# Kernel tuning notes

Measured on AMD Instinct MI355X. Metric: run time of the kernel, lower is better.

The kernel has to match this reference:

```python
import jax, jax.numpy as jnp
import numpy as np

EMBED_DIM = 2048
NUM_HEADS = 16
NUM_HEADS_KV = 16
HEAD_DIM = EMBED_DIM // NUM_HEADS  # 128
ROT_DIM = HEAD_DIM // 2            # rotary_emb_dim = 64 (partial rotary)
ROPE_BASE = 10000.0
SEQLEN = 2048


def _rope_cos_sin(seqlen):
    # inv_freq over rotary dim (fp32 positions, as pos_idx_in_fp32=True)
    inv_freq = 1.0 / (ROPE_BASE ** (jnp.arange(0, ROT_DIM, 2, dtype=jnp.float32) / ROT_DIM))
    t = jnp.arange(seqlen, dtype=jnp.float32)
    freqs = jnp.outer(t, inv_freq)                 # (S, ROT_DIM//2)
    return jnp.cos(freqs), jnp.sin(freqs)


def _apply_rotary(x, cos, sin):
    # x: (B, S, H, D); non-interleaved (GPT-NeoX) rotary on first ROT_DIM dims
    rd = cos.shape[-1] * 2
    x_rot, x_pass = x[..., :rd], x[..., rd:]
    x1, x2 = x_rot[..., : rd // 2], x_rot[..., rd // 2 :]
    c = cos[None, :, None, :]
    s = sin[None, :, None, :]
    o1 = x1 * c - x2 * s
    o2 = x1 * s + x2 * c
    return jnp.concatenate([o1, o2, x_pass], axis=-1)


def setup_inputs() -> dict:
    key = jax.random.key(0)
    ks = jax.random.split(key, 5)
    scale_in = 1.0 / np.sqrt(EMBED_DIM)
    return {
        "x_q": jax.random.normal(ks[0], (SEQLEN, EMBED_DIM), dtype=jnp.float32),
        "Wqkv_w": jax.random.normal(ks[1], (HEAD_DIM * (NUM_HEADS + 2 * NUM_HEADS_KV), EMBED_DIM), dtype=jnp.float32) * scale_in,
        "Wqkv_b": jax.random.normal(ks[2], (HEAD_DIM * (NUM_HEADS + 2 * NUM_HEADS_KV),), dtype=jnp.float32) * 0.01,
        "Wo_w": jax.random.normal(ks[3], (EMBED_DIM, EMBED_DIM), dtype=jnp.float32) * scale_in,
        "Wo_b": jax.random.normal(ks[4], (EMBED_DIM,), dtype=jnp.float32) * 0.01,
    }


def reference(x_q, Wqkv_w, Wqkv_b, Wo_w, Wo_b):
    S = x_q.shape[0]
    H, Hkv, D = NUM_HEADS, NUM_HEADS_KV, HEAD_DIM
    # fused QKV projection
    qkv = x_q @ Wqkv_w.T + Wqkv_b                     # (S, (H+2Hkv)*D)
    q = qkv[:, : H * D].reshape(1, S, H, D)
    kv = qkv[:, H * D :].reshape(1, S, 2, Hkv, D)
    # rotary (q_position_ids = k_position_ids = arange(S))
    cos, sin = _rope_cos_sin(S)
    q = _apply_rotary(q, cos, sin)
    k = _apply_rotary(kv[:, :, 0], cos, sin)          # (1, S, Hkv, D)
    v = kv[:, :, 1]
    # causal attention, softmax scale 1/sqrt(D)
    scores = jnp.einsum("bshd,bthd->bhst", q, k) / jnp.sqrt(jnp.float32(D))
    causal = jnp.arange(S)[:, None] >= jnp.arange(S)[None, :]  # (S, S)
    scores = jnp.where(causal[None, None], scores, jnp.float32(-1e30))
    attn = jax.nn.softmax(scores, axis=-1)
    out = jnp.einsum("bhst,bthd->bshd", attn, v)      # (1, S, H, D)
    out = out.reshape(1, S, H * D)
    out = out @ Wo_w.T + Wo_b
    return out[0]                                     # (S, E)
```

## Files before the change

kernel.cpp:

```cpp
#include <hip/hip_runtime.h>
#include <stdint.h>

#define QKV_N 6144
#define ATT_SCALE 0.08838834764831845f

typedef __attribute__((ext_vector_type(8))) short short8;
typedef __attribute__((ext_vector_type(4))) float f32x4;

__device__ __forceinline__ uint16_t f2b(float x){
  uint32_t u = __float_as_uint(x);
  uint32_t r = (u + 0x7fffu + ((u >> 16) & 1u)) >> 16;
  return (uint16_t)r;
}
__device__ __forceinline__ float b2f(uint16_t h){
  return __uint_as_float(((uint32_t)h) << 16);
}
__device__ __forceinline__ void g2l16(const void* g, void* l){
  __builtin_amdgcn_global_load_lds((const __attribute__((address_space(1))) void*)g,
                                   (__attribute__((address_space(3))) void*)l, 16, 0, 0);
}

__device__ __forceinline__ void cvt8(const float* __restrict__ in, uint16_t* __restrict__ out, int i){
  const float4* p = (const float4*)in;
  float4 a = p[2*i], b = p[2*i+1];
  union { short8 v; uint16_t u[8]; } o;
  o.u[0]=f2b(a.x); o.u[1]=f2b(a.y); o.u[2]=f2b(a.z); o.u[3]=f2b(a.w);
  o.u[4]=f2b(b.x); o.u[5]=f2b(b.y); o.u[6]=f2b(b.z); o.u[7]=f2b(b.w);
  ((short8*)out)[i] = o.v;
}

__global__ __launch_bounds__(256) void k_prep(const float* __restrict__ x,
                                              const float* __restrict__ wqkv,
                                              const float* __restrict__ wo,
                                              uint16_t* __restrict__ xb,
                                              uint16_t* __restrict__ wqkvb,
                                              uint16_t* __restrict__ wob,
                                              float* __restrict__ ct,
                                              float* __restrict__ st){
  const int b = blockIdx.x, tid = threadIdx.x;
  if (b < 2048) {
    cvt8(x, xb, b*256 + tid);
  } else if (b < 8192) {
    cvt8(wqkv, wqkvb, (b - 2048)*256 + tid);
  } else if (b < 10240) {
    cvt8(wo, wob, (b - 8192)*256 + tid);
  } else {
    int i = (b - 10240)*256 + tid;
    int s = i >> 5, d = i & 31;
    float inv = __expf(-(float)d * (9.210340371976184f / 32.0f));
    float f = (float)s * inv;
    ct[i] = cosf(f);
    st[i] = sinf(f);
  }
}

__global__ __launch_bounds__(512, 1) void k_gemmA(const uint16_t* __restrict__ A,
                                                  const uint16_t* __restrict__ B,
                                                  const float* __restrict__ bias,
                                                  uint16_t* __restrict__ C){
  __shared__ uint16_t As[4*4096];
  __shared__ uint16_t Bs[4*12288];
  const int K = 2048, N = 6144;

  const int wg = blockIdx.x;
  const int xcd = wg & 7, bi = wg >> 3;
  const int m0 = (xcd*2 + (bi & 1)) * 128;
  const int n0 = (bi >> 1) * 384;

  const int tid = threadIdx.x;
  const int wid = tid >> 6, l = tid & 63;
  const int wm = wid >> 2, wn = wid & 3;
  const int g = l >> 4, c = l & 15;

  const int rp_s = tid >> 3;
  const int s_s  = (tid & 7) ^ (rp_s & 7);
  const size_t srcA0 = (size_t)(m0 + rp_s*2 + (s_s >> 2)) * K + (s_s & 3) * 8;
  const size_t srcB0 = (size_t)(n0 + rp_s*2 + (s_s >> 2)) * K + (s_s & 3) * 8;
  const size_t bstride = (size_t)128 * K;

  const int pg   = ((c & 1) << 2) | g;
  const int slb  = (pg ^ ((c >> 1) & 7)) << 3;
  const int rpa0 = wm*32 + (c >> 1);
  const int rpb0 = wn*48 + (c >> 1);

  f32x4 acc[4][6] = {};
  const int NT = K >> 5;

  #pragma unroll
  for (int t0 = 0; t0 < 3; ++t0) {
    g2l16(A + srcA0 + t0*32,             (void*)(As + t0*4096  + tid*8));
    g2l16(B + srcB0 + t0*32,             (void*)(Bs + t0*12288 + tid*8));
    g2l16(B + srcB0 + bstride + t0*32,   (void*)(Bs + t0*12288 + 4096 + tid*8));
    g2l16(B + srcB0 + 2*bstride + t0*32, (void*)(Bs + t0*12288 + 8192 + tid*8));
  }
  asm volatile("s_waitcnt vmcnt(8)" ::: "memory");
  __builtin_amdgcn_s_barrier();

  #pragma unroll 4
  for (int t = 0; t < NT; ++t) {
    const uint16_t* __restrict__ Ab = As + (t & 3)*4096;
    const uint16_t* __restrict__ Bb = Bs + (t & 3)*12288;
    const int t3 = t + 3;
    const bool pf = t3 < NT;
    const int a3 = (t3 & 3)*4096;
    const int b3 = (t3 & 3)*12288;

    short8 av[4], bv[3];
    #pragma unroll
    for (int mi = 0; mi < 4; ++mi)
      av[mi] = *(const short8*)&Ab[(rpa0 + mi*8)*64 + slb];
    #pragma unroll
    for (int ni = 0; ni < 3; ++ni)
      bv[ni] = *(const short8*)&Bb[(rpb0 + ni*8)*64 + slb];
    if (pf) {
      g2l16(A + srcA0 + t3*32, (void*)(As + a3 + tid*8));
      g2l16(B + srcB0 + t3*32, (void*)(Bs + b3 + tid*8));
    }
    __builtin_amdgcn_s_barrier();
    __builtin_amdgcn_s_setprio(1);
    #pragma unroll
    for (int mi = 0; mi < 4; ++mi)
      #pragma unroll
      for (int ni = 0; ni < 3; ++ni)
        acc[mi][ni] = __builtin_amdgcn_mfma_f32_16x16x32_bf16(av[mi], bv[ni], acc[mi][ni], 0, 0, 0);
    __builtin_amdgcn_s_setprio(0);
    __builtin_amdgcn_s_barrier();

    short8 bw[3];
    #pragma unroll
    for (int ni = 0; ni < 3; ++ni)
      bw[ni] = *(const short8*)&Bb[(rpb0 + (ni+3)*8)*64 + slb];
    if (pf) {
      g2l16(B + srcB0 + bstride + t3*32,   (void*)(Bs + b3 + 4096 + tid*8));
      g2l16(B + srcB0 + 2*bstride + t3*32, (void*)(Bs + b3 + 8192 + tid*8));
    }
    __builtin_amdgcn_s_barrier();
    __builtin_amdgcn_s_setprio(1);
    #pragma unroll
    for (int mi = 0; mi < 4; ++mi)
      #pragma unroll
      for (int ni = 0; ni < 3; ++ni)
        acc[mi][ni+3] = __builtin_amdgcn_mfma_f32_16x16x32_bf16(av[mi], bw[ni], acc[mi][ni+3], 0, 0, 0);
    __builtin_amdgcn_s_setprio(0);
    asm volatile("s_waitcnt vmcnt(8)" ::: "memory");
    __builtin_amdgcn_s_barrier();
  }

  #pragma unroll
  for (int ni = 0; ni < 6; ++ni) {
    const int col = n0 + wn*96 + ni*16 + c;
    const float bvl = bias[col];
    #pragma unroll
    for (int mi = 0; mi < 4; ++mi) {
      const int row0 = m0 + wm*64 + mi*16 + g*4;
      #pragma unroll
      for (int j = 0; j < 4; ++j)
        C[(size_t)(row0 + j)*N + col] = f2b(acc[mi][ni][j] + bvl);
    }
  }
}

__global__ __launch_bounds__(512, 1) void k_gemm128(const uint16_t* __restrict__ A,
                                                    const uint16_t* __restrict__ B,
                                                    const float* __restrict__ bias,
                                                    float* __restrict__ C,
                                                    int M, int N, int K){
  __shared__ uint16_t As[4*4096];
  __shared__ uint16_t Bs[4*4096];

  const int wg = blockIdx.x;
  const int xcd = wg & 7, bi = wg >> 3;
  const int m0 = (xcd*2 + (bi & 1)) * 128;
  const int n0 = (bi >> 1) * 128;

  const int tid = threadIdx.x;
  const int wid = tid >> 6, l = tid & 63;
  const int wm = wid >> 2, wn = wid & 3;
  const int g = l >> 4, c = l & 15;

  const int rp_s = tid >> 3, q_s = tid & 7, s_s = q_s ^ (rp_s & 7);
  const int srcA = (m0 + rp_s*2 + (s_s >> 2)) * K + (s_s & 3) * 8;
  const int srcB = (n0 + rp_s*2 + (s_s >> 2)) * K + (s_s & 3) * 8;

  const int pg  = ((c & 1) << 2) | g;
  const int slb = (pg ^ ((c >> 1) & 7)) << 3;
  const int ra0 = wm*32 + (c >> 1);
  const int rb0 = wn*16 + (c >> 1);

  f32x4 acc[4][2] = {};
  const int NT = K >> 5;

  #pragma unroll
  for (int t0 = 0; t0 < 3; ++t0) {
    g2l16(A + srcA + t0*32, (void*)(As + t0*4096 + tid*8));
    g2l16(B + srcB + t0*32, (void*)(Bs + t0*4096 + tid*8));
  }
  asm volatile("s_waitcnt vmcnt(4)" ::: "memory");
  __builtin_amdgcn_s_barrier();

  #pragma unroll 4
  for (int t = 0; t < NT; ++t) {
    const uint16_t* __restrict__ Ab = As + (t & 3)*4096;
    const uint16_t* __restrict__ Bb = Bs + (t & 3)*4096;
    const int t3 = t + 3;
    const int b3 = (t3 & 3)*4096;

    short8 av[4], bv[2];
    #pragma unroll
    for (int mi = 0; mi < 4; ++mi)
      av[mi] = *(const short8*)&Ab[(ra0 + mi*8)*64 + slb];
    #pragma unroll
    for (int ni = 0; ni < 2; ++ni)
      bv[ni] = *(const short8*)&Bb[(rb0 + ni*8)*64 + slb];
    if (t3 < NT) {
      g2l16(A + srcA + t3*32, (void*)(As + b3 + tid*8));
      g2l16(B + srcB + t3*32, (void*)(Bs + b3 + tid*8));
    }
    __builtin_amdgcn_s_barrier();
    __builtin_amdgcn_s_setprio(1);
    #pragma unroll
    for (int mi = 0; mi < 4; ++mi)
      #pragma unroll
      for (int ni = 0; ni < 2; ++ni)
        acc[mi][ni] = __builtin_amdgcn_mfma_f32_16x16x32_bf16(av[mi], bv[ni], acc[mi][ni], 0, 0, 0);
    __builtin_amdgcn_s_setprio(0);
    asm volatile("s_waitcnt vmcnt(4)" ::: "memory");
    __builtin_amdgcn_s_barrier();
  }

  #pragma unroll
  for (int ni = 0; ni < 2; ++ni) {
    const int col = n0 + wn*32 + ni*16 + c;
    const float bvl = bias[col];
    #pragma unroll
    for (int mi = 0; mi < 4; ++mi) {
      const int row0 = m0 + wm*64 + mi*16 + g*4;
      #pragma unroll
      for (int j = 0; j < 4; ++j)
        C[(size_t)(row0 + j)*N + col] = acc[mi][ni][j] + bvl;
    }
  }
}

__global__ __launch_bounds__(256) void k_rope_vt(const uint16_t* __restrict__ qkv,
                                                 const float* __restrict__ ct,
                                                 const float* __restrict__ st,
                                                 uint16_t* __restrict__ qo,
                                                 uint16_t* __restrict__ ko,
                                                 uint16_t* __restrict__ vt){
  const int blk = blockIdx.x, tid = threadIdx.x;
  if (blk < 4096) {
    int idx = blk * 256 + tid;
    int db = idx & 15;
    int s  = (idx >> 4) & 2047;
    int h  = (idx >> 15) & 15;
    int which = idx >> 19;
    const uint16_t* src = qkv + (size_t)s * QKV_N + which * 2048 + h * 128;
    uint16_t* dst = (which ? ko : qo) + (((size_t)(h*2048 + s)) << 7) + db*8;
    const float scale = which ? 1.0f : ATT_SCALE;
    int d0 = db * 8;
    union { short8 v; uint16_t u[8]; } o;
    if (d0 >= 64) {
      short8 xv = *(const short8*)(src + d0);
      #pragma unroll
      for (int e = 0; e < 8; ++e) o.u[e] = f2b(b2f((uint16_t)xv[e]) * scale);
    } else {
      int dd = d0 & 31;
      short8 a = *(const short8*)(src + dd);
      short8 b = *(const short8*)(src + dd + 32);
      float4 c0 = *(const float4*)(ct + s*32 + dd);
      float4 c1 = *(const float4*)(ct + s*32 + dd + 4);
      float4 s0 = *(const float4*)(st + s*32 + dd);
      float4 s1 = *(const float4*)(st + s*32 + dd + 4);
      float cc[8] = {c0.x,c0.y,c0.z,c0.w,c1.x,c1.y,c1.z,c1.w};
      float ss[8] = {s0.x,s0.y,s0.z,s0.w,s1.x,s1.y,s1.z,s1.w};
      #pragma unroll
      for (int e = 0; e < 8; ++e) {
        float x1 = b2f((uint16_t)a[e]), x2 = b2f((uint16_t)b[e]);
        float v = (d0 < 32) ? (x1*cc[e] - x2*ss[e]) : (x1*ss[e] + x2*cc[e]);
        o.u[e] = f2b(v * scale);
      }
    }
    *(short8*)dst = o.v;
  } else {
    __shared__ uint16_t tl[64][80];
    const int b = blk - 4096;
    const int st_ = b & 31, dt = (b >> 5) & 1, h = b >> 6;
    const int s_l = tid >> 2, cch = (tid & 3) * 16;
    const uint16_t* src = qkv + (size_t)(st_*64 + s_l) * QKV_N + 4096 + h*128 + dt*64 + cch;
    short8 a = *(const short8*)src;
    short8 b2 = *(const short8*)(src + 8);
    #pragma unroll
    for (int e = 0; e < 8; ++e) {
      tl[cch + e][s_l]     = (uint16_t)a[e];
      tl[cch + 8 + e][s_l] = (uint16_t)b2[e];
    }
    __syncthreads();
    const int d_l = tid >> 2;
    uint16_t* dst = vt + ((size_t)h << 18) + (size_t)(dt*64 + d_l) * 2048 + st_*64 + cch;
    *(short8*)dst       = *(const short8*)&tl[d_l][cch];
    *(short8*)(dst + 8) = *(const short8*)&tl[d_l][cch + 8];
  }
}

__global__ __launch_bounds__(512, 1) void k_attn(const uint16_t* __restrict__ Q,
                                                 const uint16_t* __restrict__ Kb,
                                                 const uint16_t* __restrict__ Vtg,
                                                 uint16_t* __restrict__ Out){
  __shared__ uint16_t Ks[2][2][64*128];
  __shared__ uint16_t Vs[2][2][128*64];
  __shared__ uint16_t Ps[8][16*88];

  const int bid = blockIdx.x;
  const int lin = (bid & 7) * 32 + (bid >> 3);
  const int h = lin >> 4;
  const int pair = lin & 15;

  const int tid = threadIdx.x, w = tid >> 6, l = tid & 63;
  const int gid = w >> 2, wq = w & 3;
  const int tg = tid & 255;
  const int g = l >> 4, c = l & 15;
  const int swz = (c & 7) << 4;

  const uint16_t* __restrict__ Qh = Q   + ((size_t)h << 18);
  const uint16_t* __restrict__ Kh = Kb  + ((size_t)h << 18);
  const uint16_t* __restrict__ Vh = Vtg + ((size_t)h << 18);
  float* scratch = (float*)&Ks[0][0][0];

  int koff[4], voff[4];
  #pragma unroll
  for (int j = 0; j < 4; ++j) {
    int kr = j*16 + (tg >> 4);
    koff[j] = kr*128 + (((tg & 15) ^ (kr & 7)) << 3);
    int vd = j*32 + (tg >> 3);
    voff[j] = vd*2048 + (((tg & 7) ^ (vd & 7)) << 3);
  }

  uint16_t* KsG = &Ks[gid][0][0];
  uint16_t* VsG = &Vs[gid][0][0];

  #pragma unroll 1
  for (int half = 0; half < 2; ++half) {
    const int qt = half ? (31 - pair) : pair;
    const int nt = qt + 1;
    const int nsteps = (nt + 1) >> 1;
    const int qrow = qt*64 + wq*16 + c;

    short8 qf[4];
    #pragma unroll
    for (int t = 0; t < 4; ++t)
      qf[t] = *(const short8*)&Qh[(size_t)qrow*128 + t*32 + g*8];

    f32x4 acc[8] = {};
    float mrow[4], lrow[4];
    #pragma unroll
    for (int j = 0; j < 4; ++j) { mrow[j] = -3e38f; lrow[j] = 0.0f; }

    if (gid < nt) {
      #pragma unroll
      for (int j = 0; j < 4; ++j) {
        g2l16(Kh + (size_t)gid*8192 + koff[j], (void*)(KsG + j*2048 + tg*8));
        g2l16(Vh + gid*64 + voff[j],           (void*)(VsG + j*2048 + tg*8));
      }
    }
    asm volatile("s_waitcnt vmcnt(0)" ::: "memory");
    __syncthreads();

    #pragma unroll 1
    for (int step = 0; step < nsteps; ++step) {
      const int kt = 2*step + gid;
      const int cur = step & 1;
      if (kt + 2 < nt) {
        const int k1 = kt + 2;
        #pragma unroll
        for (int j = 0; j < 4; ++j) {
          g2l16(Kh + (size_t)k1*8192 + koff[j], (void*)(KsG + (cur^1)*8192 + j*2048 + tg*8));
          g2l16(Vh + k1*64 + voff[j],           (void*)(VsG + (cur^1)*8192 + j*2048 + tg*8));
        }
      }

      if (kt < nt) {
        const int k0 = kt * 64;
        const uint16_t* Kcur = KsG + cur*8192;
        const uint16_t* Vcur = VsG + cur*8192;

        f32x4 sc4[4] = {};
        #pragma unroll
        for (int ct2 = 0; ct2 < 4; ++ct2) {
          const char* krp = (const char*)Kcur + (ct2*16 + c)*256;
          #pragma unroll
          for (int t = 0; t < 4; ++t) {
            short8 kb = *(const short8*)(krp + ((t*64 + g*16) ^ swz));
            sc4[ct2] = __builtin_amdgcn_mfma_f32_16x16x32_bf16(qf[t], kb, sc4[ct2], 0, 0, 0);
          }
        }

        const bool lastt = (kt == nt - 1);
        #pragma unroll
        for (int j = 0; j < 4; ++j) {
          const int qg = qt*64 + wq*16 + g*4 + j;
          float v0 = sc4[0][j], v1 = sc4[1][j], v2 = sc4[2][j], v3 = sc4[3][j];
          if (lastt) {
            if (k0 +      c > qg) v0 = -3e38f;
            if (k0 + 16 + c > qg) v1 = -3e38f;
            if (k0 + 32 + c > qg) v2 = -3e38f;
            if (k0 + 48 + c > qg) v3 = -3e38f;
          }
          float t0 = fmaxf(fmaxf(v0, v1), fmaxf(v2, v3));
          #pragma unroll
          for (int d2 = 1; d2 < 16; d2 <<= 1) t0 = fmaxf(t0, __shfl_xor(t0, d2, 64));
          const float mn = fmaxf(mrow[j], t0);
          const float scl = __expf(mrow[j] - mn);
          const float p0 = __expf(v0 - mn), p1 = __expf(v1 - mn),
                      p2 = __expf(v2 - mn), p3 = __expf(v3 - mn);
          float rs = (p0 + p1) + (p2 + p3);
          #pragma unroll
          for (int d2 = 1; d2 < 16; d2 <<= 1) rs += __shfl_xor(rs, d2, 64);
          lrow[j] = lrow[j]*scl + rs;
          mrow[j] = mn;
          #pragma unroll
          for (int n = 0; n < 8; ++n) acc[n][j] *= scl;
          uint16_t* pw = &Ps[w][(g*4 + j)*88];
          pw[c] = f2b(p0); pw[16+c] = f2b(p1); pw[32+c] = f2b(p2); pw[48+c] = f2b(p3);
        }

        #pragma unroll
        for (int kk = 0; kk < 2; ++kk) {
          short8 pf = *(const short8*)&Ps[w][c*88 + kk*32 + g*8];
          #pragma unroll
          for (int n = 0; n < 8; ++n) {
            const char* vrp = (const char*)Vcur + (n*16 + c)*128;
            short8 vf = *(const short8*)(vrp + ((kk*64 + g*16) ^ swz));
            acc[n] = __builtin_amdgcn_mfma_f32_16x16x32_bf16(pf, vf, acc[n], 0, 0, 0);
          }
        }
      }

      asm volatile("s_waitcnt vmcnt(0)" ::: "memory");
      __syncthreads();
    }

    float* Up = scratch + wq * 2112;
    if (gid == 1) {
      #pragma unroll
      for (int j = 0; j < 4; ++j) {
        const int row = g*4 + j;
        #pragma unroll
        for (int n = 0; n < 8; ++n)
          Up[row*128 + n*16 + c] = acc[n][j];
        if (c == 0) { Up[2048 + row] = mrow[j]; Up[2064 + row] = lrow[j]; }
      }
    }
    __syncthreads();
    if (gid == 0) {
      #pragma unroll
      for (int j = 0; j < 4; ++j) {
        const int row = g*4 + j;
        const int qg = qt*64 + wq*16 + row;
        const float mB = Up[2048 + row], lB = Up[2064 + row];
        const float mn = fmaxf(mrow[j], mB);
        const float e1 = __expf(mrow[j] - mn);
        const float e2 = __expf(mB - mn);
        const float inv = 1.0f / (lrow[j]*e1 + lB*e2);
        #pragma unroll
        for (int n = 0; n < 8; ++n) {
          const float u = acc[n][j]*e1 + Up[row*128 + n*16 + c]*e2;
          Out[(size_t)qg*2048 + h*128 + n*16 + c] = f2b(u * inv);
        }
      }
    }
    __syncthreads();
  }
}

extern "C" void kernel_launch(void* const* d_in, const int* in_sizes, int n_in,
                              void* d_out, int out_size, void* d_ws, size_t ws_size,
                              hipStream_t stream){
  const float* x    = (const float*)d_in[0];
  const float* Wqkv = (const float*)d_in[1];
  const float* bqkv = (const float*)d_in[2];
  const float* Wo   = (const float*)d_in[3];
  const float* bo   = (const float*)d_in[4];

  char* ws = (char*)d_ws;
  uint16_t* q_bf    = (uint16_t*)(ws);
  uint16_t* k_bf    = (uint16_t*)(ws + 8388608);
  uint16_t* vt_bf   = (uint16_t*)(ws + 16777216);
  uint16_t* attn_bf = (uint16_t*)(ws + 25165824);
  uint16_t* x_bf    = attn_bf;
  uint16_t* wqkv_bf = (uint16_t*)(ws + 33554432);
  uint16_t* wo_bf   = (uint16_t*)(ws + 58720256);
  uint16_t* qkv_bf  = (uint16_t*)(ws + 67108864);
  float*    cos_t   = (float*)(ws + 92274688);
  float*    sin_t   = (float*)(ws + 92536832);

  k_prep<<<dim3(10496), dim3(256), 0, stream>>>(x, Wqkv, Wo, x_bf, wqkv_bf, wo_bf,
                                                cos_t, sin_t);
  k_gemmA<<<dim3(256), dim3(512), 0, stream>>>(x_bf, wqkv_bf, bqkv, qkv_bf);
  k_rope_vt<<<dim3(5120), dim3(256), 0, stream>>>(qkv_bf, cos_t, sin_t, q_bf, k_bf, vt_bf);
  k_attn<<<dim3(256), dim3(512), 0, stream>>>(q_bf, k_bf, vt_bf, attn_bf);
  k_gemm128<<<dim3(256), dim3(512), 0, stream>>>(attn_bf, wo_bf, bo, (float*)d_out,
                                                 2048, 2048, 2048);
}
```

Baseline: 173.3 us.

## Halve GEMM tile widths, double grid, and switch to triple-buffered pipelines

```diff
diff --git a/kernel.cpp b/kernel.cpp
--- a/kernel.cpp
+++ b/kernel.cpp
@@ -58,52 +58,50 @@
                                                   const uint16_t* __restrict__ B,
                                                   const float* __restrict__ bias,
                                                   uint16_t* __restrict__ C){
-  __shared__ uint16_t As[4*4096];
-  __shared__ uint16_t Bs[4*12288];
+  __shared__ uint16_t As[3*4096];
+  __shared__ uint16_t Bs[3*6144];
   const int K = 2048, N = 6144;
 
   const int wg = blockIdx.x;
   const int xcd = wg & 7, bi = wg >> 3;
   const int m0 = (xcd*2 + (bi & 1)) * 128;
-  const int n0 = (bi >> 1) * 384;
+  const int n0 = (bi >> 1) * 192;
 
   const int tid = threadIdx.x;
   const int wid = tid >> 6, l = tid & 63;
   const int wm = wid >> 2, wn = wid & 3;
   const int g = l >> 4, c = l & 15;
 
-  const int rp_s = tid >> 3;
-  const int s_s  = (tid & 7) ^ (rp_s & 7);
-  const size_t srcA0 = (size_t)(m0 + rp_s*2 + (s_s >> 2)) * K + (s_s & 3) * 8;
-  const size_t srcB0 = (size_t)(n0 + rp_s*2 + (s_s >> 2)) * K + (s_s & 3) * 8;
-  const size_t bstride = (size_t)128 * K;
+  const int rpA = tid >> 3, sA = (tid & 7) ^ (rpA & 7);
+  const size_t srcA0 = (size_t)(m0 + rpA*2 + (sA >> 2)) * K + (sA & 3) * 8;
+  const size_t srcB0 = (size_t)(n0 + rpA*2 + (sA >> 2)) * K + (sA & 3) * 8;
+  const int rpB2 = 64 + (tid >> 3), sB2 = (tid & 7) ^ (rpB2 & 7);
+  const size_t srcB1 = (size_t)(n0 + rpB2*2 + (sB2 >> 2)) * K + (sB2 & 3) * 8;
 
   const int pg   = ((c & 1) << 2) | g;
   const int slb  = (pg ^ ((c >> 1) & 7)) << 3;
   const int rpa0 = wm*32 + (c >> 1);
-  const int rpb0 = wn*48 + (c >> 1);
-
-  f32x4 acc[4][6] = {};
+  const int rpb0 = wn*24 + (c >> 1);
+
+  f32x4 acc[4][3] = {};
   const int NT = K >> 5;
 
   #pragma unroll
-  for (int t0 = 0; t0 < 3; ++t0) {
-    g2l16(A + srcA0 + t0*32,             (void*)(As + t0*4096  + tid*8));
-    g2l16(B + srcB0 + t0*32,             (void*)(Bs + t0*12288 + tid*8));
-    g2l16(B + srcB0 + bstride + t0*32,   (void*)(Bs + t0*12288 + 4096 + tid*8));
-    g2l16(B + srcB0 + 2*bstride + t0*32, (void*)(Bs + t0*12288 + 8192 + tid*8));
-  }
-  asm volatile("s_waitcnt vmcnt(8)" ::: "memory");
+  for (int t0 = 0; t0 < 2; ++t0) {
+    g2l16(A + srcA0 + t0*32, (void*)(As + t0*4096 + tid*8));
+    g2l16(B + srcB0 + t0*32, (void*)(Bs + t0*6144 + tid*8));
+    if (tid < 256)
+      g2l16(B + srcB1 + t0*32, (void*)(Bs + t0*6144 + 4096 + tid*8));
+  }
+  if (wid < 4) { asm volatile("s_waitcnt vmcnt(3)" ::: "memory"); }
+  else         { asm volatile("s_waitcnt vmcnt(2)" ::: "memory"); }
   __builtin_amdgcn_s_barrier();
 
-  #pragma unroll 4
+  #pragma unroll 3
   for (int t = 0; t < NT; ++t) {
-    const uint16_t* __restrict__ Ab = As + (t & 3)*4096;
-    const uint16_t* __restrict__ Bb = Bs + (t & 3)*12288;
-    const int t3 = t + 3;
-    const bool pf = t3 < NT;
-    const int a3 = (t3 & 3)*4096;
-    const int b3 = (t3 & 3)*12288;
+    const uint16_t* __restrict__ Ab = As + (t % 3)*4096;
+    const uint16_t* __restrict__ Bb = Bs + (t % 3)*6144;
+    const int t2 = t + 2;
 
     short8 av[4], bv[3];
     #pragma unroll
@@ -112,9 +110,12 @@
     #pragma unroll
     for (int ni = 0; ni < 3; ++ni)
       bv[ni] = *(const short8*)&Bb[(rpb0 + ni*8)*64 + slb];
-    if (pf) {
-      g2l16(A + srcA0 + t3*32, (void*)(As + a3 + tid*8));
-      g2l16(B + srcB0 + t3*32, (void*)(Bs + b3 + tid*8));
+    if (t2 < NT) {
+      const int b2 = (t2 % 3);
+      g2l16(A + srcA0 + t2*32, (void*)(As + b2*4096 + tid*8));
+      g2l16(B + srcB0 + t2*32, (void*)(Bs + b2*6144 + tid*8));
+      if (tid < 256)
+        g2l16(B + srcB1 + t2*32, (void*)(Bs + b2*6144 + 4096 + tid*8));
     }
     __builtin_amdgcn_s_barrier();
     __builtin_amdgcn_s_setprio(1);
@@ -124,31 +125,14 @@
       for (int ni = 0; ni < 3; ++ni)
         acc[mi][ni] = __builtin_amdgcn_mfma_f32_16x16x32_bf16(av[mi], bv[ni], acc[mi][ni], 0, 0, 0);
     __builtin_amdgcn_s_setprio(0);
+    if (wid < 4) { asm volatile("s_waitcnt vmcnt(3)" ::: "memory"); }
+    else         { asm volatile("s_waitcnt vmcnt(2)" ::: "memory"); }
     __builtin_amdgcn_s_barrier();
-
-    short8 bw[3];
-    #pragma unroll
-    for (int ni = 0; ni < 3; ++ni)
-      bw[ni] = *(const short8*)&Bb[(rpb0 + (ni+3)*8)*64 + slb];
-    if (pf) {
-      g2l16(B + srcB0 + bstride + t3*32,   (void*)(Bs + b3 + 4096 + tid*8));
-      g2l16(B + srcB0 + 2*bstride + t3*32, (void*)(Bs + b3 + 8192 + tid*8));
-    }
-    __builtin_amdgcn_s_barrier();
-    __builtin_amdgcn_s_setprio(1);
-    #pragma unroll
-    for (int mi = 0; mi < 4; ++mi)
-      #pragma unroll
-      for (int ni = 0; ni < 3; ++ni)
-        acc[mi][ni+3] = __builtin_amdgcn_mfma_f32_16x16x32_bf16(av[mi], bw[ni], acc[mi][ni+3], 0, 0, 0);
-    __builtin_amdgcn_s_setprio(0);
-    asm volatile("s_waitcnt vmcnt(8)" ::: "memory");
-    __builtin_amdgcn_s_barrier();
   }
 
   #pragma unroll
-  for (int ni = 0; ni < 6; ++ni) {
-    const int col = n0 + wn*96 + ni*16 + c;
+  for (int ni = 0; ni < 3; ++ni) {
+    const int col = n0 + wn*48 + ni*16 + c;
     const float bvl = bias[col];
     #pragma unroll
     for (int mi = 0; mi < 4; ++mi) {
@@ -160,27 +144,30 @@
   }
 }
 
-__global__ __launch_bounds__(512, 1) void k_gemm128(const uint16_t* __restrict__ A,
+__global__ __launch_bounds__(256, 2) void k_gemm128(const uint16_t* __restrict__ A,
                                                     const uint16_t* __restrict__ B,
                                                     const float* __restrict__ bias,
                                                     float* __restrict__ C,
                                                     int M, int N, int K){
-  __shared__ uint16_t As[4*4096];
-  __shared__ uint16_t Bs[4*4096];
+  __shared__ uint16_t As[3*4096];
+  __shared__ uint16_t Bs[3*2048];
 
   const int wg = blockIdx.x;
   const int xcd = wg & 7, bi = wg >> 3;
   const int m0 = (xcd*2 + (bi & 1)) * 128;
-  const int n0 = (bi >> 1) * 128;
+  const int n0 = (bi >> 1) * 64;
 
   const int tid = threadIdx.x;
   const int wid = tid >> 6, l = tid & 63;
-  const int wm = wid >> 2, wn = wid & 3;
+  const int wm = wid >> 1, wn = wid & 1;
   const int g = l >> 4, c = l & 15;
 
-  const int rp_s = tid >> 3, q_s = tid & 7, s_s = q_s ^ (rp_s & 7);
-  const int srcA = (m0 + rp_s*2 + (s_s >> 2)) * K + (s_s & 3) * 8;
-  const int srcB = (n0 + rp_s*2 + (s_s >> 2)) * K + (s_s & 3) * 8;
+  const int rpA1 = tid >> 3, sA1 = (tid & 7) ^ (rpA1 & 7);
+  const size_t srcA0 = (size_t)(m0 + rpA1*2 + (sA1 >> 2)) * K + (sA1 & 3) * 8;
+  const int rpA2 = 32 + (tid >> 3), sA2 = (tid & 7) ^ (rpA2 & 7);
+  const size_t srcA1 = (size_t)(m0 + rpA2*2 + (sA2 >> 2)) * K + (sA2 & 3) * 8;
+  const int rpB = tid >> 3, sB = (tid & 7) ^ (rpB & 7);
+  const size_t srcB0 = (size_t)(n0 + rpB*2 + (sB >> 2)) * K + (sB & 3) * 8;
 
   const int pg  = ((c & 1) << 2) | g;
   const int slb = (pg ^ ((c >> 1) & 7)) << 3;
@@ -191,19 +178,19 @@
   const int NT = K >> 5;
 
   #pragma unroll
-  for (int t0 = 0; t0 < 3; ++t0) {
-    g2l16(A + srcA + t0*32, (void*)(As + t0*4096 + tid*8));
-    g2l16(B + srcB + t0*32, (void*)(Bs + t0*4096 + tid*8));
-  }
-  asm volatile("s_waitcnt vmcnt(4)" ::: "memory");
+  for (int t0 = 0; t0 < 2; ++t0) {
+    g2l16(A + srcA0 + t0*32, (void*)(As + t0*4096 + tid*8));
+    g2l16(A + srcA1 + t0*32, (void*)(As + t0*4096 + 2048 + tid*8));
+    g2l16(B + srcB0 + t0*32, (void*)(Bs + t0*2048 + tid*8));
+  }
+  asm volatile("s_waitcnt vmcnt(3)" ::: "memory");
   __builtin_amdgcn_s_barrier();
 
-  #pragma unroll 4
+  #pragma unroll 3
   for (int t = 0; t < NT; ++t) {
-    const uint16_t* __restrict__ Ab = As + (t & 3)*4096;
-    const uint16_t* __restrict__ Bb = Bs + (t & 3)*4096;
-    const int t3 = t + 3;
-    const int b3 = (t3 & 3)*4096;
+    const uint16_t* __restrict__ Ab = As + (t % 3)*4096;
+    const uint16_t* __restrict__ Bb = Bs + (t % 3)*2048;
+    const int t2 = t + 2;
 
     short8 av[4], bv[2];
     #pragma unroll
@@ -212,9 +199,11 @@
     #pragma unroll
     for (int ni = 0; ni < 2; ++ni)
       bv[ni] = *(const short8*)&Bb[(rb0 + ni*8)*64 + slb];
-    if (t3 < NT) {
-      g2l16(A + srcA + t3*32, (void*)(As + b3 + tid*8));
-      g2l16(B + srcB + t3*32, (void*)(Bs + b3 + tid*8));
+    if (t2 < NT) {
+      const int b2 = (t2 % 3);
+      g2l16(A + srcA0 + t2*32, (void*)(As + b2*4096 + tid*8));
+      g2l16(A + srcA1 + t2*32, (void*)(As + b2*4096 + 2048 + tid*8));
+      g2l16(B + srcB0 + t2*32, (void*)(Bs + b2*2048 + tid*8));
     }
     __builtin_amdgcn_s_barrier();
     __builtin_amdgcn_s_setprio(1);
@@ -224,7 +213,7 @@
       for (int ni = 0; ni < 2; ++ni)
         acc[mi][ni] = __builtin_amdgcn_mfma_f32_16x16x32_bf16(av[mi], bv[ni], acc[mi][ni], 0, 0, 0);
     __builtin_amdgcn_s_setprio(0);
-    asm volatile("s_waitcnt vmcnt(4)" ::: "memory");
+    asm volatile("s_waitcnt vmcnt(3)" ::: "memory");
     __builtin_amdgcn_s_barrier();
   }
 
@@ -496,9 +485,9 @@
 
   k_prep<<<dim3(10496), dim3(256), 0, stream>>>(x, Wqkv, Wo, x_bf, wqkv_bf, wo_bf,
                                                 cos_t, sin_t);
-  k_gemmA<<<dim3(256), dim3(512), 0, stream>>>(x_bf, wqkv_bf, bqkv, qkv_bf);
+  k_gemmA<<<dim3(512), dim3(512), 0, stream>>>(x_bf, wqkv_bf, bqkv, qkv_bf);
   k_rope_vt<<<dim3(5120), dim3(256), 0, stream>>>(qkv_bf, cos_t, sin_t, q_bf, k_bf, vt_bf);
   k_attn<<<dim3(256), dim3(512), 0, stream>>>(q_bf, k_bf, vt_bf, attn_bf);
-  k_gemm128<<<dim3(256), dim3(512), 0, stream>>>(attn_bf, wo_bf, bo, (float*)d_out,
+  k_gemm128<<<dim3(512), dim3(256), 0, stream>>>(attn_bf, wo_bf, bo, (float*)d_out,
                                                  2048, 2048, 2048);
 }
```

Measured after the change: 175.8 us. About the same (+1.5%).
